# Kernel tuning notes

Measured on AMD Instinct MI355X. Metric: run time of the kernel, lower is better.

## Reference

```python
import jax, jax.numpy as jnp
import numpy as np

B, S, D_MODEL, D_HIDDEN = 4, 2048, 1024, 4096

# --- BitNet b1.58-style quantizers (STE in bwd version) ---

def act_quant(x):
    # per-token int8 absmax quantization over last dim
    scale = 127.0 / jnp.clip(jnp.max(jnp.abs(x), axis=-1, keepdims=True), 1e-5)
    return jnp.clip(jnp.round(x * scale), -128, 127) / scale

def weight_quant(w):
    # ternary weights with global mean-abs scale
    scale = 1.0 / jnp.clip(jnp.mean(jnp.abs(w)), 1e-5)
    return jnp.clip(jnp.round(w * scale), -1, 1) / scale

def bit_linear(x, w):
    # STE: forward uses quantized values, gradient passes through
    xq = x + jax.lax.stop_gradient(act_quant(x) - x)
    wq = w + jax.lax.stop_gradient(weight_quant(w) - w)
    return jnp.einsum('bsd,hd->bsh', xq, wq)

def depthwise_conv1d(x_bcl, w, b):
    # x_bcl: [B, C, L], w: [C, 1, 3], b: [C]
    y = jax.lax.conv_general_dilated(
        x_bcl, w, window_strides=(1,), padding=[(1, 1)],
        dimension_numbers=('NCH', 'OIH', 'NCH'),
        feature_group_count=x_bcl.shape[1])
    return y + b[None, :, None]


def setup_inputs() -> dict:
    key = jax.random.key(0)
    ks = jax.random.split(key, 5)
    lim1 = 1.0 / np.sqrt(D_MODEL)
    lim2 = 1.0 / np.sqrt(D_HIDDEN)
    limc = 1.0 / np.sqrt(3.0)  # fan_in = 1*3 for depthwise conv
    return {
        'x': jax.random.normal(ks[0], (B, S, D_MODEL), dtype=jnp.float32),
        'w1': jax.random.uniform(ks[1], (D_HIDDEN, D_MODEL), jnp.float32, -lim1, lim1),
        'conv_w': jax.random.uniform(ks[2], (D_HIDDEN, 1, 3), jnp.float32, -limc, limc),
        'conv_b': jax.random.uniform(ks[3], (D_HIDDEN,), jnp.float32, -limc, limc),
        'w2': jax.random.uniform(ks[4], (D_MODEL, D_HIDDEN), jnp.float32, -lim2, lim2),
    }


def reference(x, w1, conv_w, conv_b, w2):
    h = bit_linear(x, w1)                      # [B, S, H]
    h = depthwise_conv1d(h.transpose(0, 2, 1), conv_w, conv_b)  # [B, H, S]
    h = h.transpose(0, 2, 1)                   # [B, S, H]
    h = jax.nn.silu(h)
    return bit_linear(h, w2)                   # [B, S, D]
```

## Files before the change

kernel.cpp:

```cpp
#include <hip/hip_runtime.h>
#include <cstdint>

#define S_    2048
#define DM    1024
#define DH    4096
#define NTOK  8192
#define WELEM 4194304
#define CT    8

typedef int v4i __attribute__((ext_vector_type(4)));
typedef _Float16 half8 __attribute__((ext_vector_type(8)));
typedef char char8v __attribute__((ext_vector_type(8)));

#define GLOAD_LDS16(g, l)                                                   \
    __builtin_amdgcn_global_load_lds(                                       \
        (const __attribute__((address_space(1))) void*)(g),                 \
        (__attribute__((address_space(3))) void*)(l), 16, 0, 0)

static __device__ __forceinline__ void sbar() {
    asm volatile("" ::: "memory");
    __builtin_amdgcn_s_barrier();
    asm volatile("" ::: "memory");
}
#define LGKM0() asm volatile("s_waitcnt lgkmcnt(0)" ::: "memory")
#define VMC6()  asm volatile("s_waitcnt vmcnt(6)" ::: "memory")
#define VMC0()  asm volatile("s_waitcnt vmcnt(0)" ::: "memory")

__global__ __launch_bounds__(256) void absmean_partial(const float4* __restrict__ wa,
                                                       const float4* __restrict__ wb,
                                                       double* __restrict__ partial) {
    __shared__ double red[256];
    const float4* w = (blockIdx.x < 1024) ? wa : wb;
    int base = (blockIdx.x & 1023) * 1024;
    double s = 0.0;
#pragma unroll
    for (int k = 0; k < 4; ++k) {
        float4 v = w[base + (k << 8) + threadIdx.x];
        s += (double)fabsf(v.x) + (double)fabsf(v.y) +
             (double)fabsf(v.z) + (double)fabsf(v.w);
    }
    red[threadIdx.x] = s;
    __syncthreads();
    for (int off = 128; off > 0; off >>= 1) {
        if (threadIdx.x < off) red[threadIdx.x] += red[threadIdx.x + off];
        __syncthreads();
    }
    if (threadIdx.x == 0) partial[blockIdx.x] = red[0];
}

__global__ __launch_bounds__(256) void finalize_scales(const double* __restrict__ part,
                                                       float* __restrict__ sc) {
    __shared__ double red[1024];
#pragma unroll 1
    for (int m = 0; m < 2; ++m) {
        const double* p = part + m * 1024;
        __syncthreads();
#pragma unroll
        for (int k = 0; k < 4; ++k) red[(k << 8) + threadIdx.x] = p[(k << 8) + threadIdx.x];
        __syncthreads();
        double s = red[threadIdx.x] + red[threadIdx.x + 256] +
                   red[threadIdx.x + 512] + red[threadIdx.x + 768];
        __syncthreads();
        red[threadIdx.x] = s;
        __syncthreads();
        for (int off = 128; off > 0; off >>= 1) {
            if (threadIdx.x < off) red[threadIdx.x] += red[threadIdx.x + off];
            __syncthreads();
        }
        if (threadIdx.x == 0) {
            double mean = red[0] / (double)WELEM;
            float mf = fmaxf((float)mean, 1e-5f);
            float scale = 1.0f / mf;
            sc[2 * m]     = scale;
            sc[2 * m + 1] = 1.0f / scale;
        }
    }
}

__global__ __launch_bounds__(256) void quant_all(const float4* __restrict__ w1,
                                                 const float4* __restrict__ w2,
                                                 const float4* __restrict__ x,
                                                 char4* __restrict__ qw1,
                                                 char4* __restrict__ qw2,
                                                 char4* __restrict__ qx,
                                                 float* __restrict__ dqx,
                                                 const float* __restrict__ sc) {
    __shared__ float red[256];
    if (blockIdx.x < 8192) {
        bool second = blockIdx.x >= 4096;
        const float4* w = second ? w2 : w1;
        char4* q = second ? qw2 : qw1;
        float scale = sc[second ? 2 : 0];
        int i = (blockIdx.x & 4095) * 256 + threadIdx.x;
        float4 v = w[i];
        char4 o;
        o.x = (signed char)(int)fminf(fmaxf(rintf(v.x * scale), -1.f), 1.f);
        o.y = (signed char)(int)fminf(fmaxf(rintf(v.y * scale), -1.f), 1.f);
        o.z = (signed char)(int)fminf(fmaxf(rintf(v.z * scale), -1.f), 1.f);
        o.w = (signed char)(int)fminf(fmaxf(rintf(v.w * scale), -1.f), 1.f);
        q[i] = o;
    } else {
        int t = blockIdx.x - 8192;
        float4 v = x[(size_t)t * 256 + threadIdx.x];
        float mx = fmaxf(fmaxf(fabsf(v.x), fabsf(v.y)), fmaxf(fabsf(v.z), fabsf(v.w)));
        red[threadIdx.x] = mx;
        __syncthreads();
        for (int off = 128; off > 0; off >>= 1) {
            if (threadIdx.x < off) red[threadIdx.x] = fmaxf(red[threadIdx.x], red[threadIdx.x + off]);
            __syncthreads();
        }
        float scale = 127.0f / fmaxf(red[0], 1e-5f);
        char4 o;
        o.x = (signed char)(int)fminf(fmaxf(rintf(v.x * scale), -128.f), 127.f);
        o.y = (signed char)(int)fminf(fmaxf(rintf(v.y * scale), -128.f), 127.f);
        o.z = (signed char)(int)fminf(fmaxf(rintf(v.z * scale), -128.f), 127.f);
        o.w = (signed char)(int)fminf(fmaxf(rintf(v.w * scale), -128.f), 127.f);
        qx[(size_t)t * 256 + threadIdx.x] = o;
        if (threadIdx.x == 0) dqx[t] = 1.0f / scale;
    }
}

__global__ __launch_bounds__(512) void conv_silu_quant(const half8* __restrict__ h,
                                                       const float4* __restrict__ cwv,
                                                       const float4* __restrict__ cbv,
                                                       char8v* __restrict__ q,
                                                       float* __restrict__ dq) {
    __shared__ float red[2][8];
    const int tid = threadIdx.x;
    const int t0 = blockIdx.x * CT;
    const int s0 = t0 & (S_ - 1);

    float wc[24], bs[8];
    {
        float4 tmp;
#pragma unroll
        for (int i = 0; i < 6; ++i) {
            tmp = cwv[tid * 6 + i];
            wc[4 * i] = tmp.x; wc[4 * i + 1] = tmp.y; wc[4 * i + 2] = tmp.z; wc[4 * i + 3] = tmp.w;
        }
        tmp = cbv[tid * 2];     bs[0] = tmp.x; bs[1] = tmp.y; bs[2] = tmp.z; bs[3] = tmp.w;
        tmp = cbv[tid * 2 + 1]; bs[4] = tmp.x; bs[5] = tmp.y; bs[6] = tmp.z; bs[7] = tmp.w;
    }

    auto ldrow = [&](int t, bool valid, float* dst) {
        if (valid) {
            half8 raw = h[(size_t)t * 512 + tid];
#pragma unroll
            for (int e = 0; e < 8; ++e) dst[e] = (float)raw[e];
        } else {
#pragma unroll
            for (int e = 0; e < 8; ++e) dst[e] = 0.f;
        }
    };

    float pv[8], cu[8], nx[8], pf[8];
    ldrow(t0 - 1, s0 > 0, pv);
    ldrow(t0, true, cu);
    ldrow(t0 + 1, true, nx);

#pragma unroll
    for (int i = 0; i < CT; ++i) {
        const int t = t0 + i;
        ldrow(t + 2, (s0 + i + 2) < S_, pf);

        float v[8];
        float mx = 0.f;
#pragma unroll
        for (int e = 0; e < 8; ++e) {
            float y = wc[3 * e] * pv[e] + wc[3 * e + 1] * cu[e] + wc[3 * e + 2] * nx[e] + bs[e];
            float r = y / (1.0f + expf(-y));
            v[e] = r;
            mx = fmaxf(mx, fabsf(r));
        }
#pragma unroll
        for (int off = 32; off > 0; off >>= 1)
            mx = fmaxf(mx, __shfl_down(mx, off, 64));
        if ((tid & 63) == 0) red[i & 1][tid >> 6] = mx;
        __syncthreads();
        float rmax = red[i & 1][0];
#pragma unroll
        for (int w = 1; w < 8; ++w) rmax = fmaxf(rmax, red[i & 1][w]);
        float scale = 127.0f / fmaxf(rmax, 1e-5f);
        char8v o;
#pragma unroll
        for (int e = 0; e < 8; ++e)
            o[e] = (signed char)(int)fminf(fmaxf(rintf(v[e] * scale), -128.f), 127.f);
        q[(size_t)t * 512 + tid] = o;
        if (tid == 0) dq[t] = 1.0f / scale;
#pragma unroll
        for (int e = 0; e < 8; ++e) { pv[e] = cu[e]; cu[e] = nx[e]; nx[e] = pf[e]; }
    }
}

template <typename OutT>
__global__ __launch_bounds__(512, 2) void gemm_i8_3s(const int8_t* __restrict__ A,
                                                     const int8_t* __restrict__ Bm,
                                                     OutT* __restrict__ C,
                                                     const float* __restrict__ rowdq,
                                                     const float* __restrict__ sc, int slot,
                                                     int N, int K) {
    __shared__ __align__(16) int8_t lds[3][49152];
    const int tid  = threadIdx.x;
    const int lane = tid & 63;
    const int wave = tid >> 6;
    const int mbase = blockIdx.y << 8;
    const int nbase = blockIdx.x << 7;
    const int NT = K >> 7;

    const int wm = wave >> 1;
    const int wn = wave & 1;

    const int srow  = tid >> 3;
    const int lchnk = (tid & 7) ^ (srow & 7);
    const int8_t* Ag = A  + (size_t)(mbase + srow) * K + (lchnk << 4);
    const int8_t* Bg = Bm + (size_t)(nbase + srow) * K + (lchnk << 4);
    const size_t rstep = (size_t)64 * K;

    auto stage = [&](int s, int t, int half) {
        const size_t ko = (size_t)t << 7;
        int8_t* db = &lds[s][wave << 10];
        if (half == 0) {
            GLOAD_LDS16(Ag + ko,               db);
            GLOAD_LDS16(Ag + ko + rstep,       db + 8192);
            GLOAD_LDS16(Ag + ko + 2 * rstep,   db + 16384);
        } else {
            GLOAD_LDS16(Ag + ko + 3 * rstep,   db + 24576);
            GLOAD_LDS16(Bg + ko,               db + 32768);
            GLOAD_LDS16(Bg + ko + rstep,       db + 40960);
        }
    };

    const int fc0 = (((lane >> 4)    ) ^ (lane & 7)) << 4;
    const int fc1 = (((lane >> 4) | 4) ^ (lane & 7)) << 4;
    const int aro = ((wm << 6) + (lane & 15)) << 7;
    const int bro = 32768 + (((wn << 6) + (lane & 15)) << 7);

    v4i acc[4][4] = {};

    stage(0, 0, 0); stage(0, 0, 1);
    if (NT > 1) { stage(1, 1, 0); stage(1, 1, 1); }
    if (NT > 1) VMC6(); else VMC0();
    sbar();

    int sb = 0;
    for (int t = 0; t < NT; ++t) {
        const int8_t* base = &lds[sb][0];
        int s2 = sb + 2; if (s2 >= 3) s2 -= 3;

        v4i af[4], bf[4];
#pragma unroll
        for (int i = 0; i < 4; ++i)
            af[i] = *reinterpret_cast<const v4i*>(base + aro + (i << 11) + fc0);
#pragma unroll
        for (int j = 0; j < 4; ++j)
            bf[j] = *reinterpret_cast<const v4i*>(base + bro + (j << 11) + fc0);
        if (t + 2 < NT) stage(s2, t + 2, 0);
        sbar();
        LGKM0();
        __builtin_amdgcn_s_setprio(1);
#pragma unroll
        for (int i = 0; i < 4; ++i)
#pragma unroll
            for (int j = 0; j < 4; ++j)
                acc[i][j] = __builtin_amdgcn_mfma_i32_16x16x64_i8(af[i], bf[j], acc[i][j], 0, 0, 0);
        __builtin_amdgcn_s_setprio(0);
        sbar();

#pragma unroll
        for (int i = 0; i < 4; ++i)
            af[i] = *reinterpret_cast<const v4i*>(base + aro + (i << 11) + fc1);
#pragma unroll
        for (int j = 0; j < 4; ++j)
            bf[j] = *reinterpret_cast<const v4i*>(base + bro + (j << 11) + fc1);
        if (t + 2 < NT) stage(s2, t + 2, 1);
        sbar();
        LGKM0();
        __builtin_amdgcn_s_setprio(1);
#pragma unroll
        for (int i = 0; i < 4; ++i)
#pragma unroll
            for (int j = 0; j < 4; ++j)
                acc[i][j] = __builtin_amdgcn_mfma_i32_16x16x64_i8(af[i], bf[j], acc[i][j], 0, 0, 0);
        __builtin_amdgcn_s_setprio(0);
        if (t + 2 < NT)      VMC6();
        else if (t + 1 < NT) VMC0();
        sbar();

        if (++sb == 3) sb = 0;
    }

    const float wdq = sc[slot];
    const int quad = lane >> 4;
    const int col  = lane & 15;
#pragma unroll
    for (int i = 0; i < 4; ++i) {
#pragma unroll
        for (int r = 0; r < 4; ++r) {
            int m = mbase + (wm << 6) + (i << 4) + (quad << 2) + r;
            float rs = rowdq[m] * wdq;
#pragma unroll
            for (int j = 0; j < 4; ++j) {
                int n = nbase + (wn << 6) + (j << 4) + col;
                C[(size_t)m * N + n] = (OutT)((float)acc[i][j][r] * rs);
            }
        }
    }
}

extern "C" void kernel_launch(void* const* d_in, const int* in_sizes, int n_in,
                              void* d_out, int out_size, void* d_ws, size_t ws_size,
                              hipStream_t stream) {
    const float* x  = (const float*)d_in[0];
    const float* w1 = (const float*)d_in[1];
    const float* cw = (const float*)d_in[2];
    const float* cb = (const float*)d_in[3];
    const float* w2 = (const float*)d_in[4];
    float* out = (float*)d_out;
    char* ws = (char*)d_ws;

    double* part  = (double*)(ws + 0);
    float*  sc    = (float*)(ws + 16384);
    float*  dqx   = (float*)(ws + 16640);
    float*  dqh   = (float*)(ws + 49408);
    int8_t* qw1   = (int8_t*)(ws + 82176);
    int8_t* qw2   = (int8_t*)(ws + 4276480);
    int8_t* qx    = (int8_t*)(ws + 8470784);
    int8_t* qh    = (int8_t*)(ws + 16859392);
    _Float16* h   = (_Float16*)(ws + 50413824);

    absmean_partial<<<2048, 256, 0, stream>>>((const float4*)w1, (const float4*)w2, part);
    finalize_scales<<<1, 256, 0, stream>>>(part, sc);
    quant_all<<<16384, 256, 0, stream>>>((const float4*)w1, (const float4*)w2,
                                         (const float4*)x, (char4*)qw1, (char4*)qw2,
                                         (char4*)qx, dqx, sc);

    dim3 g1(DH / 128, NTOK / 256);
    gemm_i8_3s<_Float16><<<g1, 512, 0, stream>>>(qx, qw1, h, dqx, sc, 1, DH, DM);

    conv_silu_quant<<<NTOK / CT, 512, 0, stream>>>((const half8*)h, (const float4*)cw,
                                                   (const float4*)cb, (char8v*)qh, dqh);

    dim3 g2(DM / 128, NTOK / 256);
    gemm_i8_3s<float><<<g2, 512, 0, stream>>>(qh, qw2, out, dqh, sc, 3, DM, DH);
}
```

Measured before the change: 257.5 us.

## Rework int8 GEMM to BK=64 stages with grid swizzle and smaller second tile

```diff
diff --git a/kernel.cpp b/kernel.cpp
--- a/kernel.cpp
+++ b/kernel.cpp
@@ -22,9 +22,9 @@
     __builtin_amdgcn_s_barrier();
     asm volatile("" ::: "memory");
 }
-#define LGKM0() asm volatile("s_waitcnt lgkmcnt(0)" ::: "memory")
-#define VMC6()  asm volatile("s_waitcnt vmcnt(6)" ::: "memory")
-#define VMC0()  asm volatile("s_waitcnt vmcnt(0)" ::: "memory")
+#define VMC0() asm volatile("s_waitcnt vmcnt(0)" ::: "memory")
+#define VMC3() asm volatile("s_waitcnt vmcnt(3)" ::: "memory")
+#define VMC4() asm volatile("s_waitcnt vmcnt(4)" ::: "memory")
 
 __global__ __launch_bounds__(256) void absmean_partial(const float4* __restrict__ wa,
                                                        const float4* __restrict__ wb,
@@ -192,71 +192,76 @@
     }
 }
 
-template <typename OutT>
-__global__ __launch_bounds__(512, 2) void gemm_i8_3s(const int8_t* __restrict__ A,
-                                                     const int8_t* __restrict__ Bm,
-                                                     OutT* __restrict__ C,
-                                                     const float* __restrict__ rowdq,
-                                                     const float* __restrict__ sc, int slot,
-                                                     int N, int K) {
-    __shared__ __align__(16) int8_t lds[3][49152];
+template <int BM, int WAVES, typename OutT>
+__global__ __launch_bounds__(WAVES * 64, (BM == 256) ? 4 : 3)
+void gemm_i8_bk64(const int8_t* __restrict__ A, const int8_t* __restrict__ Bm,
+                  OutT* __restrict__ C, const float* __restrict__ rowdq,
+                  const float* __restrict__ sc, int slot, int N, int K) {
+    constexpr int BN = 128;
+    constexpr int ABYTES = BM * 64;
+    constexpr int BUF = (BM + BN) * 64;
+    constexpr int ALOADS = BM / 16 / WAVES;
+    constexpr int BLOADS = BN / 16 / WAVES;
+    constexpr int L = ALOADS + BLOADS;
+
+    __shared__ __align__(16) int8_t lds[3][BUF];
     const int tid  = threadIdx.x;
     const int lane = tid & 63;
     const int wave = tid >> 6;
-    const int mbase = blockIdx.y << 8;
-    const int nbase = blockIdx.x << 7;
-    const int NT = K >> 7;
+
+    const int nwg = gridDim.x * gridDim.y;
+    int flat = blockIdx.y * gridDim.x + blockIdx.x;
+    flat = (flat & 7) * (nwg >> 3) + (flat >> 3);
+    const int bx = flat % gridDim.x;
+    const int by = flat / gridDim.x;
+    const int mbase = by * BM;
+    const int nbase = bx << 7;
+    const int NT = K >> 6;
 
     const int wm = wave >> 1;
     const int wn = wave & 1;
 
-    const int srow  = tid >> 3;
-    const int lchnk = (tid & 7) ^ (srow & 7);
-    const int8_t* Ag = A  + (size_t)(mbase + srow) * K + (lchnk << 4);
-    const int8_t* Bg = Bm + (size_t)(nbase + srow) * K + (lchnk << 4);
-    const size_t rstep = (size_t)64 * K;
-
-    auto stage = [&](int s, int t, int half) {
-        const size_t ko = (size_t)t << 7;
-        int8_t* db = &lds[s][wave << 10];
-        if (half == 0) {
-            GLOAD_LDS16(Ag + ko,               db);
-            GLOAD_LDS16(Ag + ko + rstep,       db + 8192);
-            GLOAD_LDS16(Ag + ko + 2 * rstep,   db + 16384);
-        } else {
-            GLOAD_LDS16(Ag + ko + 3 * rstep,   db + 24576);
-            GLOAD_LDS16(Bg + ko,               db + 32768);
-            GLOAD_LDS16(Bg + ko + rstep,       db + 40960);
-        }
+    const int srow = lane >> 2;
+    const int csrc = (((lane & 3) ^ ((lane >> 3) & 3)) << 4);
+    const int8_t* Ag = A  + (size_t)(mbase + wave * (ALOADS * 16) + srow) * K + csrc;
+    const int8_t* Bg = Bm + (size_t)(nbase + wave * (BLOADS * 16) + srow) * K + csrc;
+
+    auto stage = [&](int s, int tt) {
+        const size_t ko = (size_t)tt << 6;
+        int8_t* dA = &lds[s][(wave * ALOADS) << 10];
+        int8_t* dB = &lds[s][ABYTES + ((wave * BLOADS) << 10)];
+#pragma unroll
+        for (int l = 0; l < ALOADS; ++l)
+            GLOAD_LDS16(Ag + ko + (size_t)(l * 16) * K, dA + (l << 10));
+#pragma unroll
+        for (int l = 0; l < BLOADS; ++l)
+            GLOAD_LDS16(Bg + ko + (size_t)(l * 16) * K, dB + (l << 10));
     };
 
-    const int fc0 = (((lane >> 4)    ) ^ (lane & 7)) << 4;
-    const int fc1 = (((lane >> 4) | 4) ^ (lane & 7)) << 4;
-    const int aro = ((wm << 6) + (lane & 15)) << 7;
-    const int bro = 32768 + (((wn << 6) + (lane & 15)) << 7);
+    const int fc   = (((lane >> 4) ^ ((lane >> 1) & 3)) << 4);
+    const int aoff = ((wm * 64 + (lane & 15)) << 6) + fc;
+    const int boff = ABYTES + ((wn * 64 + (lane & 15)) << 6) + fc;
 
     v4i acc[4][4] = {};
 
-    stage(0, 0, 0); stage(0, 0, 1);
-    if (NT > 1) { stage(1, 1, 0); stage(1, 1, 1); }
-    if (NT > 1) VMC6(); else VMC0();
+    stage(0, 0);
+    stage(1, 1);
+    if constexpr (L == 3) VMC3(); else VMC4();
     sbar();
 
     int sb = 0;
     for (int t = 0; t < NT; ++t) {
         const int8_t* base = &lds[sb][0];
+        v4i af[4], bf[4];
+#pragma unroll
+        for (int i = 0; i < 4; ++i)
+            af[i] = *reinterpret_cast<const v4i*>(base + aoff + (i << 10));
+#pragma unroll
+        for (int j = 0; j < 4; ++j)
+            bf[j] = *reinterpret_cast<const v4i*>(base + boff + (j << 10));
         int s2 = sb + 2; if (s2 >= 3) s2 -= 3;
-
-        v4i af[4], bf[4];
-#pragma unroll
-        for (int i = 0; i < 4; ++i)
-            af[i] = *reinterpret_cast<const v4i*>(base + aro + (i << 11) + fc0);
-#pragma unroll
-        for (int j = 0; j < 4; ++j)
-            bf[j] = *reinterpret_cast<const v4i*>(base + bro + (j << 11) + fc0);
-        if (t + 2 < NT) stage(s2, t + 2, 0);
-        sbar();
-        LGKM0();
+        if (t + 2 < NT) stage(s2, t + 2);
+
         __builtin_amdgcn_s_setprio(1);
 #pragma unroll
         for (int i = 0; i < 4; ++i)
@@ -264,28 +269,10 @@
             for (int j = 0; j < 4; ++j)
                 acc[i][j] = __builtin_amdgcn_mfma_i32_16x16x64_i8(af[i], bf[j], acc[i][j], 0, 0, 0);
         __builtin_amdgcn_s_setprio(0);
-        sbar();
-
-#pragma unroll
-        for (int i = 0; i < 4; ++i)
-            af[i] = *reinterpret_cast<const v4i*>(base + aro + (i << 11) + fc1);
-#pragma unroll
-        for (int j = 0; j < 4; ++j)
-            bf[j] = *reinterpret_cast<const v4i*>(base + bro + (j << 11) + fc1);
-        if (t + 2 < NT) stage(s2, t + 2, 1);
-        sbar();
-        LGKM0();
-        __builtin_amdgcn_s_setprio(1);
-#pragma unroll
-        for (int i = 0; i < 4; ++i)
-#pragma unroll
-            for (int j = 0; j < 4; ++j)
-                acc[i][j] = __builtin_amdgcn_mfma_i32_16x16x64_i8(af[i], bf[j], acc[i][j], 0, 0, 0);
-        __builtin_amdgcn_s_setprio(0);
-        if (t + 2 < NT)      VMC6();
+
+        if (t + 2 < NT)      { if constexpr (L == 3) VMC3(); else VMC4(); }
         else if (t + 1 < NT) VMC0();
         sbar();
-
         if (++sb == 3) sb = 0;
     }
 
@@ -335,11 +322,11 @@
                                          (char4*)qx, dqx, sc);
 
     dim3 g1(DH / 128, NTOK / 256);
-    gemm_i8_3s<_Float16><<<g1, 512, 0, stream>>>(qx, qw1, h, dqx, sc, 1, DH, DM);
+    gemm_i8_bk64<256, 8, _Float16><<<g1, 512, 0, stream>>>(qx, qw1, h, dqx, sc, 1, DH, DM);
 
     conv_silu_quant<<<NTOK / CT, 512, 0, stream>>>((const half8*)h, (const float4*)cw,
                                                    (const float4*)cb, (char8v*)qh, dqh);
 
-    dim3 g2(DM / 128, NTOK / 256);
-    gemm_i8_3s<float><<<g2, 512, 0, stream>>>(qh, qw2, out, dqh, sc, 3, DM, DH);
-}
+    dim3 g2(DM / 128, NTOK / 128);
+    gemm_i8_bk64<128, 4, float><<<g2, 256, 0, stream>>>(qh, qw2, out, dqh, sc, 3, DM, DH);
+}
```

Measured after the change: 247.1 us. -4.0%, faster.
